# Performance work log

Measured on AMD Instinct MI355X. Metric: run time of the kernel, lower is better.

## Reference

```python
import jax, jax.numpy as jnp
import numpy as np

# static graph/layer sizes
N_SRC0, N_DST0 = 60000, 15000
N_DST1 = 4000
H1, D1 = 8, 256   # layer1: 8 heads, 256 per head
H2, D2 = 1, 128   # layer2: 1 head, 128 (= out_feats)
IN_DIM = H1 * D1  # 2048


def gat_conv(feat, W, al, ar, b, src, dst, n_dst, H, D, act):
    # feat: [N_src, F]; W: [F, H*D]; al/ar: [H, D]; b: [H*D]
    h = (feat @ W).reshape(feat.shape[0], H, D)          # [N_src, H, D]
    el = jnp.einsum('nhd,hd->nh', h, al)                 # [N_src, H]
    er = jnp.einsum('nhd,hd->nh', h[:n_dst], ar)         # [N_dst, H]
    e = jax.nn.leaky_relu(el[src] + er[dst], 0.2)        # [E, H]
    # edge softmax grouped by destination node (numerically stable)
    emax = jax.ops.segment_max(e, dst, num_segments=n_dst)
    emax = jnp.where(jnp.isfinite(emax), emax, 0.0)      # guard zero-in-degree dsts
    ex = jnp.exp(e - emax[dst])
    denom = jax.ops.segment_sum(ex, dst, num_segments=n_dst)
    a = ex / denom[dst]                                  # [E, H]
    out = jax.ops.segment_sum(h[src] * a[:, :, None], dst, num_segments=n_dst)
    out = out + b.reshape(1, H, D)
    return jax.nn.relu(out) if act else out              # [N_dst, H, D]


def setup_inputs() -> dict:
    key = jax.random.key(0)
    ks = jax.random.split(key, 16)
    feat = jax.random.normal(ks[0], (N_SRC0, IN_DIM), dtype=jnp.float32)
    src0 = jax.random.randint(ks[1], (240000,), 0, N_SRC0, dtype=jnp.int32)
    dst0 = jax.random.randint(ks[2], (240000,), 0, N_DST0, dtype=jnp.int32)
    src1 = jax.random.randint(ks[3], (64000,), 0, N_DST0, dtype=jnp.int32)
    dst1 = jax.random.randint(ks[4], (64000,), 0, N_DST1, dtype=jnp.int32)
    # layer1 params (in 2048 -> 8 heads x 256)
    W1 = jax.random.normal(ks[5], (IN_DIM, H1 * D1), dtype=jnp.float32) / np.sqrt(IN_DIM)
    al1 = jax.random.normal(ks[6], (H1, D1), dtype=jnp.float32) / np.sqrt(D1)
    ar1 = jax.random.normal(ks[7], (H1, D1), dtype=jnp.float32) / np.sqrt(D1)
    b1 = jnp.zeros((H1 * D1,), dtype=jnp.float32)
    # layer2 params (in 256 (post head-mean) -> 1 head x 128)
    W2 = jax.random.normal(ks[8], (D1, H2 * D2), dtype=jnp.float32) / np.sqrt(D1)
    al2 = jax.random.normal(ks[9], (H2, D2), dtype=jnp.float32) / np.sqrt(D2)
    ar2 = jax.random.normal(ks[10], (H2, D2), dtype=jnp.float32) / np.sqrt(D2)
    b2 = jnp.zeros((H2 * D2,), dtype=jnp.float32)
    return {"feat": feat, "W1": W1, "al1": al1, "ar1": ar1, "b1": b1,
            "W2": W2, "al2": al2, "ar2": ar2, "b2": b2,
            "src0": src0, "dst0": dst0, "src1": src1, "dst1": dst1}


def reference(feat, W1, al1, ar1, b1, W2, al2, ar2, b2, src0, dst0, src1, dst1):
    h = gat_conv(feat, W1, al1, ar1, b1, src0, dst0, N_DST0, H1, D1, act=True)
    h = h.mean(axis=1)                                   # head mean -> [N_DST0, 256]
    h = gat_conv(h, W2, al2, ar2, b2, src1, dst1, N_DST1, H2, D2, act=False)
    return h.reshape(N_DST1, H2 * D2)                    # flatten(1) -> [4000, 128]
```

## Files before the change

kernel.cpp:

```cpp
#include <hip/hip_runtime.h>
#include <hip/hip_bf16.h>


typedef __bf16 bf16;
typedef bf16 bf16x8 __attribute__((ext_vector_type(8)));
typedef float f32x4 __attribute__((ext_vector_type(4)));

#define N_SRC0V 60000
#define N_DST0V 15000
#define N_DST1V 4000
#define E0V 240000
#define E1V 64000
#define HD1V 2048
#define K1V 2048
#define M1PAD 60160
#define M2PAD 15104

#define BM 128
#define BN 128
#define BK 64

#define GBM 256
#define GBN 256
#define GBK 64

__device__ __forceinline__ void gload16(const void* g, void* l) {
  __builtin_amdgcn_global_load_lds(
      (__attribute__((address_space(1))) void*)(g),
      (__attribute__((address_space(3))) void*)(l), 16, 0, 0);
}

__global__ void k_convert(const float* __restrict__ x, bf16* __restrict__ y, long n8) {
  long i = (long)blockIdx.x * 256 + threadIdx.x;
  if (i >= n8) return;
  const float4* xp = (const float4*)(x + i * 8);
  float4 a = xp[0], b = xp[1];
  bf16x8 o;
  o[0] = (bf16)a.x; o[1] = (bf16)a.y; o[2] = (bf16)a.z; o[3] = (bf16)a.w;
  o[4] = (bf16)b.x; o[5] = (bf16)b.y; o[6] = (bf16)b.z; o[7] = (bf16)b.w;
  *(bf16x8*)(y + i * 8) = o;
}

__global__ void k_transpose_bf16(const float* __restrict__ W, bf16* __restrict__ WT,
                                 int R, int C) {
  __shared__ float tile[32][33];
  int tx = threadIdx.x & 31, ty = threadIdx.x >> 5;
  int c0 = blockIdx.x * 32, r0 = blockIdx.y * 32;
  for (int i = ty; i < 32; i += 8) {
    int r = r0 + i, c = c0 + tx;
    tile[i][tx] = (r < R && c < C) ? W[(size_t)r * C + c] : 0.f;
  }
  __syncthreads();
  for (int i = ty; i < 32; i += 8) {
    int c = c0 + i, r = r0 + tx;
    if (c < C && r < R) WT[(size_t)c * R + r] = (bf16)tile[tx][i];
  }
}

__global__ __launch_bounds__(512, 2) void k_gemm256_bt(
    const bf16* __restrict__ A, const bf16* __restrict__ BT,
    bf16* __restrict__ C, int N, int K) {
  extern __shared__ char smem_raw[];
  bf16* smem = (bf16*)smem_raw;
  const int tid = threadIdx.x;
  const int lane = tid & 63;
  const int wv = tid >> 6;
  const int wm = wv >> 2;
  const int wn = wv & 3;
  const int lr = lane & 15, lq = lane >> 4;

  int nwg = gridDim.x * gridDim.y;
  int flat = blockIdx.y * gridDim.x + blockIdx.x;
  if ((nwg & 7) == 0) {
    int cpx = nwg >> 3;
    flat = (flat & 7) * cpx + (flat >> 3);
  }
  const int m0 = (flat / gridDim.x) * GBM;
  const int n0 = (flat % gridDim.x) * GBN;

  const f32x4 vzero = {0.f, 0.f, 0.f, 0.f};
  f32x4 acc[8][4];
#pragma unroll
  for (int i = 0; i < 8; ++i)
#pragma unroll
    for (int j = 0; j < 4; ++j) acc[i][j] = vzero;

  auto stage = [&](int b, int k0) {
    bf16* sAb = smem + b * 32768;
    bf16* sBb = sAb + 16384;
#pragma unroll
    for (int it = 0; it < 4; ++it) {
      int c = it * 512 + tid;
      int seg = c >> 6;
      int ln = c & 63;
      int row = (seg >> 1) * 16 + (ln & 15);
      int col = (seg & 1) * 32 + (ln >> 4) * 8;
      gload16(A + (size_t)(m0 + row) * K + k0 + col, &sAb[c * 8]);
      gload16(BT + (size_t)(n0 + row) * K + k0 + col, &sBb[c * 8]);
    }
  };

  const int NT = K / GBK;
  stage(0, 0);
  __syncthreads();

  for (int kt = 0; kt < NT; ++kt) {
    const int cur = kt & 1;
    bf16* sAb = smem + cur * 32768;
    bf16* sBb = sAb + 16384;
    if (kt + 1 < NT) stage(cur ^ 1, (kt + 1) * GBK);
#pragma unroll
    for (int kb = 0; kb < 2; ++kb) {
      bf16x8 af[8], bfr[4];
#pragma unroll
      for (int i = 0; i < 8; ++i)
        af[i] = *(const bf16x8*)&sAb[(((wm * 8 + i) * 2 + kb) * 64 + lane) * 8];
#pragma unroll
      for (int j = 0; j < 4; ++j)
        bfr[j] = *(const bf16x8*)&sBb[(((wn * 4 + j) * 2 + kb) * 64 + lane) * 8];
      __builtin_amdgcn_s_setprio(1);
#pragma unroll
      for (int i = 0; i < 8; ++i)
#pragma unroll
        for (int j = 0; j < 4; ++j)
          acc[i][j] = __builtin_amdgcn_mfma_f32_16x16x32_bf16(af[i], bfr[j], acc[i][j], 0, 0, 0);
      __builtin_amdgcn_s_setprio(0);
    }
    __syncthreads();
  }

#pragma unroll
  for (int i = 0; i < 8; ++i)
#pragma unroll
    for (int j = 0; j < 4; ++j) {
      int row = m0 + wm * 128 + i * 16 + lq * 4;
      int col = n0 + wn * 64 + j * 16 + lr;
#pragma unroll
      for (int r = 0; r < 4; ++r)
        C[(size_t)(row + r) * N + col] = (bf16)acc[i][j][r];
    }
}

template <typename OutT>
__global__ __launch_bounds__(256) void k_gemm_bt(
    const bf16* __restrict__ A, const bf16* __restrict__ BT,
    OutT* __restrict__ C, int N, int K) {
  __shared__ bf16 sA[BM * BK];
  __shared__ bf16 sB[BN * BK];
  const int tid = threadIdx.x;
  const int lane = tid & 63;
  const int wv = tid >> 6;
  const int wm = wv >> 1, wn = wv & 1;
  const int lr = lane & 15, lq = lane >> 4;
  const int m0 = blockIdx.y * BM;
  const int n0 = blockIdx.x * BN;

  const f32x4 vzero = {0.f, 0.f, 0.f, 0.f};
  f32x4 acc[4][4];
#pragma unroll
  for (int i = 0; i < 4; ++i)
#pragma unroll
    for (int j = 0; j < 4; ++j) acc[i][j] = vzero;

  for (int k0 = 0; k0 < K; k0 += BK) {
#pragma unroll
    for (int it = 0; it < 4; ++it) {
      int c = it * 256 + tid;
      int seg = c >> 6;
      int ln = c & 63;
      int row = (seg >> 1) * 16 + (ln & 15);
      int col = (seg & 1) * 32 + (ln >> 4) * 8;
      gload16(A + (size_t)(m0 + row) * K + k0 + col, &sA[c * 8]);
      gload16(BT + (size_t)(n0 + row) * K + k0 + col, &sB[c * 8]);
    }
    __syncthreads();
#pragma unroll
    for (int kk = 0; kk < BK; kk += 32) {
      const int kb = kk >> 5;
      bf16x8 af[4], bfr[4];
#pragma unroll
      for (int i = 0; i < 4; ++i)
        af[i] = *(const bf16x8*)&sA[(((wm * 4 + i) * 2 + kb) * 64 + lane) * 8];
#pragma unroll
      for (int j = 0; j < 4; ++j)
        bfr[j] = *(const bf16x8*)&sB[(((wn * 4 + j) * 2 + kb) * 64 + lane) * 8];
#pragma unroll
      for (int i = 0; i < 4; ++i)
#pragma unroll
        for (int j = 0; j < 4; ++j)
          acc[i][j] = __builtin_amdgcn_mfma_f32_16x16x32_bf16(af[i], bfr[j], acc[i][j], 0, 0, 0);
    }
    __syncthreads();
  }
#pragma unroll
  for (int i = 0; i < 4; ++i)
#pragma unroll
    for (int j = 0; j < 4; ++j) {
      int row = m0 + wm * 64 + i * 16 + lq * 4;
      int col = n0 + wn * 64 + j * 16 + lr;
#pragma unroll
      for (int r = 0; r < 4; ++r)
        C[(size_t)(row + r) * N + col] = (OutT)acc[i][j][r];
    }
}

__global__ void k_el_er1(const bf16* __restrict__ h, const float* __restrict__ al,
                         const float* __restrict__ ar, float* __restrict__ el,
                         float* __restrict__ er, int n_dst) {
  int row = blockIdx.x;
  int t = threadIdx.x;
  bf16x8 hv = *(const bf16x8*)(h + (size_t)row * 2048 + t * 8);
  float pl = 0.f, pr = 0.f;
#pragma unroll
  for (int e = 0; e < 8; ++e) {
    float v = (float)hv[e];
    pl += v * al[t * 8 + e];
    pr += v * ar[t * 8 + e];
  }
#pragma unroll
  for (int off = 16; off >= 1; off >>= 1) {
    pl += __shfl_down(pl, off);
    pr += __shfl_down(pr, off);
  }
  if ((t & 31) == 0) {
    el[(size_t)row * 8 + (t >> 5)] = pl;
    if (row < n_dst) er[(size_t)row * 8 + (t >> 5)] = pr;
  }
}

__global__ void k_el_er2(const float* __restrict__ h, const float* __restrict__ al,
                         const float* __restrict__ ar, float* __restrict__ el,
                         float* __restrict__ er, int n_el, int n_dst) {
  int t = threadIdx.x;
  int row = blockIdx.x * 16 + (t >> 4);
  int s = t & 15;
  const float* hp = h + (size_t)row * 128 + s * 8;
  float4 a = *(const float4*)hp;
  float4 b = *(const float4*)(hp + 4);
  float pl = a.x * al[s * 8] + a.y * al[s * 8 + 1] + a.z * al[s * 8 + 2] + a.w * al[s * 8 + 3]
           + b.x * al[s * 8 + 4] + b.y * al[s * 8 + 5] + b.z * al[s * 8 + 6] + b.w * al[s * 8 + 7];
  float pr = a.x * ar[s * 8] + a.y * ar[s * 8 + 1] + a.z * ar[s * 8 + 2] + a.w * ar[s * 8 + 3]
           + b.x * ar[s * 8 + 4] + b.y * ar[s * 8 + 5] + b.z * ar[s * 8 + 6] + b.w * ar[s * 8 + 7];
#pragma unroll
  for (int off = 8; off >= 1; off >>= 1) {
    pl += __shfl_down(pl, off);
    pr += __shfl_down(pr, off);
  }
  if (s == 0 && row < n_el) {
    el[row] = pl;
    if (row < n_dst) er[row] = pr;
  }
}

__global__ void k_zero(int* __restrict__ p, int n) {
  int i = blockIdx.x * 256 + threadIdx.x;
  if (i < n) p[i] = 0;
}
__global__ void k_hist(const int* __restrict__ d, int E, int* __restrict__ counts) {
  int e = blockIdx.x * 256 + threadIdx.x;
  if (e < E) atomicAdd(&counts[d[e]], 1);
}
__global__ void k_scan(const int* __restrict__ counts, int n, int* __restrict__ offs,
                       int* __restrict__ cursor) {
  __shared__ int part[1024];
  int t = threadIdx.x;
  int per = (n + 1023) >> 10;
  int b = t * per;
  int e = b + per < n ? b + per : n;
  int s = 0;
  for (int i = b; i < e; ++i) s += counts[i];
  part[t] = s;
  __syncthreads();
  for (int off = 1; off < 1024; off <<= 1) {
    int v = 0;
    if (t >= off) v = part[t - off];
    __syncthreads();
    part[t] += v;
    __syncthreads();
  }
  int run = (t == 0) ? 0 : part[t - 1];
  for (int i = b; i < e; ++i) { offs[i] = run; cursor[i] = run; run += counts[i]; }
  if (t == 1023) offs[n] = run;
}
__global__ void k_scatter(const int* __restrict__ d, int E, int* __restrict__ cursor,
                          int* __restrict__ eperm) {
  int e = blockIdx.x * 256 + threadIdx.x;
  if (e < E) eperm[atomicAdd(&cursor[d[e]], 1)] = e;
}

__global__ void k_stats(const int* __restrict__ offs, const int* __restrict__ eperm,
                        const int* __restrict__ srcv, const float* __restrict__ el,
                        const float* __restrict__ er, int n_dst, int H,
                        float* __restrict__ emax, float* __restrict__ eden) {
  int idx = blockIdx.x * 256 + threadIdx.x;
  if (idx >= n_dst * H) return;
  int dn = idx / H, hh = idx - dn * H;
  int s0 = offs[dn], s1 = offs[dn + 1];
  float erv = er[idx];
  float mx = -1e30f;
  for (int p = s0; p < s1; ++p) {
    float v = el[srcv[eperm[p]] * H + hh] + erv;
    v = v > 0.f ? v : 0.2f * v;
    mx = fmaxf(mx, v);
  }
  if (s1 == s0) mx = 0.f;
  float s = 0.f;
  for (int p = s0; p < s1; ++p) {
    float v = el[srcv[eperm[p]] * H + hh] + erv;
    v = v > 0.f ? v : 0.2f * v;
    s += expf(v - mx);
  }
  emax[idx] = mx;
  eden[idx] = s;
}

__global__ __launch_bounds__(256) void k_aggr1(
    const int* __restrict__ offs, const int* __restrict__ eperm,
    const int* __restrict__ srcv, const float* __restrict__ el,
    const float* __restrict__ er, const float* __restrict__ emax,
    const float* __restrict__ eden, const bf16* __restrict__ h1,
    const float* __restrict__ b1, bf16* __restrict__ outm) {
  int dn = blockIdx.x;
  int t = threadIdx.x;
  int head = t >> 5;
  int jd = (t & 31) << 3;
  __shared__ float wbuf[32][8];
  __shared__ int sidx[32];
  __shared__ float obuf[2048];
  float acc[8] = {0.f, 0.f, 0.f, 0.f, 0.f, 0.f, 0.f, 0.f};
  int s0 = offs[dn], s1 = offs[dn + 1];
  for (int base = s0; base < s1; base += 32) {
    int rem = s1 - base;
    int cnt = rem < 32 ? rem : 32;
    __syncthreads();
    if (t < cnt * 8) {
      int ec = t >> 3, hh = t & 7;
      int e = eperm[base + ec];
      int sv = srcv[e];
      if (hh == 0) sidx[ec] = sv;
      float v = el[sv * 8 + hh] + er[dn * 8 + hh];
      v = v > 0.f ? v : 0.2f * v;
      float den = eden[dn * 8 + hh];
      wbuf[ec][hh] = den > 0.f ? expf(v - emax[dn * 8 + hh]) / den : 0.f;
    }
    __syncthreads();
    for (int ec = 0; ec < cnt; ++ec) {
      float w = wbuf[ec][head];
      const bf16* hp = h1 + (size_t)sidx[ec] * 2048 + (head << 8) + jd;
      bf16x8 x = *(const bf16x8*)hp;
#pragma unroll
      for (int e2 = 0; e2 < 8; ++e2) acc[e2] += w * (float)x[e2];
    }
  }
  int ob = (head << 8) + jd;
#pragma unroll
  for (int k2 = 0; k2 < 8; ++k2) {
    float v = acc[k2] + b1[ob + k2];
    obuf[ob + k2] = v > 0.f ? v : 0.f;
  }
  __syncthreads();
  float sum = 0.f;
#pragma unroll
  for (int hh = 0; hh < 8; ++hh) sum += obuf[hh * 256 + t];
  outm[(size_t)dn * 256 + t] = (bf16)(sum * 0.125f);
}

__global__ __launch_bounds__(128) void k_aggr2(
    const int* __restrict__ offs, const int* __restrict__ eperm,
    const int* __restrict__ srcv, const float* __restrict__ el,
    const float* __restrict__ er, const float* __restrict__ emax,
    const float* __restrict__ eden, const float* __restrict__ h2,
    const float* __restrict__ b2, float* __restrict__ out) {
  int dn = blockIdx.x;
  int t = threadIdx.x;
  __shared__ float wbuf[64];
  __shared__ int sidx[64];
  float acc = 0.f;
  int s0 = offs[dn], s1 = offs[dn + 1];
  float erv = er[dn], mx = emax[dn], den = eden[dn];
  for (int base = s0; base < s1; base += 64) {
    int rem = s1 - base;
    int cnt = rem < 64 ? rem : 64;
    __syncthreads();
    if (t < cnt) {
      int e = eperm[base + t];
      int sv = srcv[e];
      sidx[t] = sv;
      float v = el[sv] + erv;
      v = v > 0.f ? v : 0.2f * v;
      wbuf[t] = den > 0.f ? expf(v - mx) / den : 0.f;
    }
    __syncthreads();
    for (int ec = 0; ec < cnt; ++ec)
      acc += wbuf[ec] * h2[(size_t)sidx[ec] * 128 + t];
  }
  out[(size_t)dn * 128 + t] = acc + b2[t];
}

extern "C" void kernel_launch(void* const* d_in, const int* in_sizes, int n_in,
                              void* d_out, int out_size, void* d_ws, size_t ws_size,
                              hipStream_t stream) {
  const float* feat = (const float*)d_in[0];
  const float* W1   = (const float*)d_in[1];
  const float* al1  = (const float*)d_in[2];
  const float* ar1  = (const float*)d_in[3];
  const float* b1   = (const float*)d_in[4];
  const float* W2   = (const float*)d_in[5];
  const float* al2  = (const float*)d_in[6];
  const float* ar2  = (const float*)d_in[7];
  const float* b2   = (const float*)d_in[8];
  const int* src0   = (const int*)d_in[9];
  const int* dst0   = (const int*)d_in[10];
  const int* src1   = (const int*)d_in[11];
  const int* dst1   = (const int*)d_in[12];
  float* out = (float*)d_out;

  static bool s_attr_set = false;
  if (!s_attr_set) {
    hipFuncSetAttribute(reinterpret_cast<const void*>(k_gemm256_bt),
                        hipFuncAttributeMaxDynamicSharedMemorySize, 131072);
    s_attr_set = true;
  }

  char* w = (char*)d_ws;
  auto alloc = [&](size_t bytes) {
    char* p = w;
    w += (bytes + 255) & ~(size_t)255;
    return p;
  };
  bf16*  featb   = (bf16*)alloc((size_t)M1PAD * K1V * 2);
  bf16*  w1t     = (bf16*)alloc((size_t)HD1V * K1V * 2);
  bf16*  w2t     = (bf16*)alloc((size_t)128 * 256 * 2);
  bf16*  h1      = (bf16*)alloc((size_t)M1PAD * HD1V * 2);
  float* el1     = (float*)alloc((size_t)N_SRC0V * 8 * 4);
  float* er1     = (float*)alloc((size_t)N_DST0V * 8 * 4);
  float* emax1   = (float*)alloc((size_t)N_DST0V * 8 * 4);
  float* eden1   = (float*)alloc((size_t)N_DST0V * 8 * 4);
  bf16*  outm    = (bf16*)alloc((size_t)M2PAD * 256 * 2);
  float* h2      = (float*)alloc((size_t)M2PAD * 128 * 4);
  float* el2     = (float*)alloc((size_t)N_DST0V * 4);
  float* er2     = (float*)alloc((size_t)N_DST1V * 4);
  float* emax2   = (float*)alloc((size_t)N_DST1V * 4);
  float* eden2   = (float*)alloc((size_t)N_DST1V * 4);
  int*   counts1 = (int*)alloc((size_t)N_DST0V * 4);
  int*   offs1   = (int*)alloc((size_t)(N_DST0V + 1) * 4);
  int*   cursor1 = (int*)alloc((size_t)N_DST0V * 4);
  int*   eperm1  = (int*)alloc((size_t)E0V * 4);
  int*   counts2 = (int*)alloc((size_t)N_DST1V * 4);
  int*   offs2   = (int*)alloc((size_t)(N_DST1V + 1) * 4);
  int*   cursor2 = (int*)alloc((size_t)N_DST1V * 4);
  int*   eperm2  = (int*)alloc((size_t)E1V * 4);

  k_zero<<<(N_DST0V + 255) / 256, 256, 0, stream>>>(counts1, N_DST0V);
  k_zero<<<(N_DST1V + 255) / 256, 256, 0, stream>>>(counts2, N_DST1V);
  {
    long n8 = (long)N_SRC0V * K1V / 8;
    k_convert<<<(unsigned)((n8 + 255) / 256), 256, 0, stream>>>(feat, featb, n8);
    int padi = (M1PAD - N_SRC0V) * K1V / 2;
    k_zero<<<(padi + 255) / 256, 256, 0, stream>>>(
        (int*)(featb + (size_t)N_SRC0V * K1V), padi);
  }
  k_transpose_bf16<<<dim3(64, 64), 256, 0, stream>>>(W1, w1t, K1V, HD1V);
  k_transpose_bf16<<<dim3(4, 8), 256, 0, stream>>>(W2, w2t, 256, 128);

  k_gemm256_bt<<<dim3(HD1V / GBN, M1PAD / GBM), 512, 131072, stream>>>(
      featb, w1t, h1, HD1V, K1V);
  k_el_er1<<<N_SRC0V, 256, 0, stream>>>(h1, al1, ar1, el1, er1, N_DST0V);
  k_hist<<<(E0V + 255) / 256, 256, 0, stream>>>(dst0, E0V, counts1);
  k_scan<<<1, 1024, 0, stream>>>(counts1, N_DST0V, offs1, cursor1);
  k_scatter<<<(E0V + 255) / 256, 256, 0, stream>>>(dst0, E0V, cursor1, eperm1);
  k_stats<<<(N_DST0V * 8 + 255) / 256, 256, 0, stream>>>(offs1, eperm1, src0, el1, er1,
                                                         N_DST0V, 8, emax1, eden1);
  k_aggr1<<<N_DST0V, 256, 0, stream>>>(offs1, eperm1, src0, el1, er1, emax1, eden1,
                                       h1, b1, outm);

  k_gemm_bt<float><<<dim3(1, M2PAD / BM), 256, 0, stream>>>(outm, w2t, h2, 128, 256);
  k_el_er2<<<M2PAD / 16, 256, 0, stream>>>(h2, al2, ar2, el2, er2, N_DST0V, N_DST1V);
  k_hist<<<(E1V + 255) / 256, 256, 0, stream>>>(dst1, E1V, counts2);
  k_scan<<<1, 1024, 0, stream>>>(counts2, N_DST1V, offs2, cursor2);
  k_scatter<<<(E1V + 255) / 256, 256, 0, stream>>>(dst1, E1V, cursor2, eperm2);
  k_stats<<<(N_DST1V + 255) / 256, 256, 0, stream>>>(offs2, eperm2, src1, el2, er2,
                                                     N_DST1V, 1, emax2, eden2);
  k_aggr2<<<N_DST1V, 128, 0, stream>>>(offs2, eperm2, src1, el2, er2, emax2, eden2,
                                       h2, b2, out);
}
```

Measured before the change: 1.694 ms.

## Deepen GEMM LDS pipeline to four stages with explicit vmcnt waits

```diff
diff --git a/kernel.cpp b/kernel.cpp
--- a/kernel.cpp
+++ b/kernel.cpp
@@ -22,7 +22,7 @@
 
 #define GBM 256
 #define GBN 256
-#define GBK 64
+#define GBK 32
 
 __device__ __forceinline__ void gload16(const void* g, void* l) {
   __builtin_amdgcn_global_load_lds(
@@ -86,47 +86,67 @@
     for (int j = 0; j < 4; ++j) acc[i][j] = vzero;
 
   auto stage = [&](int b, int k0) {
-    bf16* sAb = smem + b * 32768;
-    bf16* sBb = sAb + 16384;
-#pragma unroll
-    for (int it = 0; it < 4; ++it) {
+    bf16* sAb = smem + b * 16384;
+    bf16* sBb = sAb + 8192;
+#pragma unroll
+    for (int it = 0; it < 2; ++it) {
       int c = it * 512 + tid;
-      int seg = c >> 6;
       int ln = c & 63;
-      int row = (seg >> 1) * 16 + (ln & 15);
-      int col = (seg & 1) * 32 + (ln >> 4) * 8;
+      int row = (c >> 6) * 16 + (ln & 15);
+      int col = (ln >> 4) * 8;
       gload16(A + (size_t)(m0 + row) * K + k0 + col, &sAb[c * 8]);
+    }
+#pragma unroll
+    for (int it = 0; it < 2; ++it) {
+      int c = it * 512 + tid;
+      int ln = c & 63;
+      int row = (c >> 6) * 16 + (ln & 15);
+      int col = (ln >> 4) * 8;
       gload16(BT + (size_t)(n0 + row) * K + k0 + col, &sBb[c * 8]);
     }
   };
 
   const int NT = K / GBK;
   stage(0, 0);
-  __syncthreads();
+  stage(1, GBK);
+  stage(2, 2 * GBK);
 
   for (int kt = 0; kt < NT; ++kt) {
-    const int cur = kt & 1;
-    bf16* sAb = smem + cur * 32768;
-    bf16* sBb = sAb + 16384;
-    if (kt + 1 < NT) stage(cur ^ 1, (kt + 1) * GBK);
-#pragma unroll
-    for (int kb = 0; kb < 2; ++kb) {
-      bf16x8 af[8], bfr[4];
-#pragma unroll
-      for (int i = 0; i < 8; ++i)
-        af[i] = *(const bf16x8*)&sAb[(((wm * 8 + i) * 2 + kb) * 64 + lane) * 8];
+    const int cb = kt & 3;
+    const bf16* sAb = smem + cb * 16384;
+    const bf16* sBb = sAb + 8192;
+
+    if (kt < NT - 2) {
+      asm volatile("s_waitcnt vmcnt(8)" ::: "memory");
+    } else if (kt == NT - 2) {
+      asm volatile("s_waitcnt vmcnt(4)" ::: "memory");
+    } else {
+      asm volatile("s_waitcnt vmcnt(0)" ::: "memory");
+    }
+    __builtin_amdgcn_sched_barrier(0);
+    __builtin_amdgcn_s_barrier();
+    __builtin_amdgcn_sched_barrier(0);
+
+    if (kt + 3 < NT) stage((kt + 3) & 3, (kt + 3) * GBK);
+
+    bf16x8 af[8], bfr[4];
+#pragma unroll
+    for (int j = 0; j < 4; ++j)
+      bfr[j] = *(const bf16x8*)&sBb[((wn * 4 + j) * 64 + lane) * 8];
+#pragma unroll
+    for (int i = 0; i < 8; ++i)
+      af[i] = *(const bf16x8*)&sAb[((wm * 8 + i) * 64 + lane) * 8];
+    __builtin_amdgcn_sched_barrier(0);
+    asm volatile("s_waitcnt lgkmcnt(0)" ::: "memory");
+    __builtin_amdgcn_sched_barrier(0);
+    __builtin_amdgcn_s_setprio(1);
+#pragma unroll
+    for (int i = 0; i < 8; ++i)
 #pragma unroll
       for (int j = 0; j < 4; ++j)
-        bfr[j] = *(const bf16x8*)&sBb[(((wn * 4 + j) * 2 + kb) * 64 + lane) * 8];
-      __builtin_amdgcn_s_setprio(1);
-#pragma unroll
-      for (int i = 0; i < 8; ++i)
-#pragma unroll
-        for (int j = 0; j < 4; ++j)
-          acc[i][j] = __builtin_amdgcn_mfma_f32_16x16x32_bf16(af[i], bfr[j], acc[i][j], 0, 0, 0);
-      __builtin_amdgcn_s_setprio(0);
-    }
-    __syncthreads();
+        acc[i][j] = __builtin_amdgcn_mfma_f32_16x16x32_bf16(af[i], bfr[j], acc[i][j], 0, 0, 0);
+    __builtin_amdgcn_s_setprio(0);
+    __builtin_amdgcn_sched_barrier(0);
   }
 
 #pragma unroll
```

Measured after the change: 1.604 ms. -5.3%, faster.
